# Performance work log

Measured on AMD Instinct MI355X. Metric: run time of the kernel, lower is better.

Reference implementation:

```python
import jax, jax.numpy as jnp
import numpy as np

NUM_BINS = 20
EMBED_DIM = 768
NUM_CODES = 1000
BATCH = 131072
EPS = 1e-8


def setup_inputs() -> dict:
    key = jax.random.key(0)
    k1, k2, k3, k4 = jax.random.split(key, 4)
    values = jax.random.uniform(k1, (BATCH,), dtype=jnp.float32)
    code_ids = jax.random.randint(k2, (BATCH,), 0, NUM_CODES, dtype=jnp.int32)
    # per-code sorted quantile boundaries, shape (NUM_CODES, NUM_BINS-1)
    boundaries = jnp.sort(
        jax.random.uniform(k3, (NUM_CODES, NUM_BINS - 1), dtype=jnp.float32), axis=1
    )
    embed_table = jax.random.normal(k4, (NUM_BINS, EMBED_DIM), dtype=jnp.float32)
    return {
        "values": values,
        "code_ids": code_ids,
        "boundaries": boundaries,
        "embed_table": embed_table,
    }


def reference(values, code_ids, boundaries, embed_table):
    nb = embed_table.shape[0]  # num_bins
    # gather each sample's boundary row: (B, nb-1)
    brows = boundaries[code_ids]
    # torch.searchsorted default == side='left'
    idx = jax.vmap(jnp.searchsorted)(brows, values)
    idx = jnp.clip(idx, 0, nb - 1)
    interior = (idx > 0) & (idx < nb - 1)
    # boundary gathers (clipped so edge rows stay in range; masked out below)
    lo_b = jnp.take_along_axis(brows, jnp.clip(idx - 1, 0, nb - 2)[:, None], axis=1)[:, 0]
    hi_b = jnp.take_along_axis(brows, jnp.clip(idx, 0, nb - 2)[:, None], axis=1)[:, 0]
    denom = hi_b - lo_b
    tiny = jnp.abs(denom) < EPS
    safe_denom = jnp.where(tiny, 1.0, denom)
    alpha = jnp.where(tiny, 0.5, jnp.clip((values - lo_b) / safe_denom, 0.0, 1.0))
    # at edge bins the original returns a single bin embedding (alpha irrelevant)
    alpha = jnp.where(interior, alpha, 0.0)
    lower_idx = jnp.where(idx == 0, 0, jnp.where(idx >= nb - 1, nb - 1, idx - 1))
    upper_idx = jnp.where(interior, idx, lower_idx)
    a = alpha[:, None]
    out = (1.0 - a) * embed_table[lower_idx] + a * embed_table[upper_idx]
    return out  # (B, EMBED_DIM)
```

## Files before the change

kernel.cpp:

```cpp
#include <hip/hip_runtime.h>
#include <cfloat>

#define NB      20
#define NBOUND  19
#define ED      768
#define ED4     192
#define EPS     1e-8f

__global__ __launch_bounds__(256) void sde_kernel(
    const float* __restrict__ values,
    const int*   __restrict__ code_ids,
    const float* __restrict__ boundaries,
    const float* __restrict__ embed_table,
    float*       __restrict__ out,
    int batch)
{
    const int wave = blockIdx.x * (blockDim.x >> 6) + (threadIdx.x >> 6);
    const int lane = threadIdx.x & 63;
    if (wave >= batch) return;
    const int b = wave;

    const float v = values[b];
    const int   c = code_ids[b];

    float bnd = FLT_MAX;
    if (lane < NBOUND) bnd = boundaries[(size_t)c * NBOUND + lane];

    const unsigned long long lt = __ballot(bnd < v);
    const int idx = __popcll(lt);

    int lo_i = idx - 1; lo_i = lo_i < 0 ? 0 : lo_i;
    int hi_i = idx > NBOUND - 1 ? NBOUND - 1 : idx;
    const float lo_b = __shfl(bnd, lo_i);
    const float hi_b = __shfl(bnd, hi_i);

    const bool interior = (idx > 0) && (idx < NB - 1);
    const float denom = hi_b - lo_b;
    const bool tiny = fabsf(denom) < EPS;

    float alpha = (v - lo_b) / (tiny ? 1.0f : denom);
    alpha = fminf(fmaxf(alpha, 0.0f), 1.0f);
    if (tiny)      alpha = 0.5f;
    if (!interior) alpha = 0.0f;

    const int lower = (idx == 0) ? 0 : ((idx >= NB - 1) ? NB - 1 : idx - 1);
    const int upper = interior ? idx : lower;

    const float4* __restrict__ tlo = (const float4*)(embed_table + (size_t)lower * ED);
    const float4* __restrict__ thi = (const float4*)(embed_table + (size_t)upper * ED);
    float4* __restrict__ orow = (float4*)(out + (size_t)b * ED);

    const float om = 1.0f - alpha;
    #pragma unroll
    for (int k = 0; k < 3; ++k) {
        const int s = lane + k * 64;
        const float4 e0 = tlo[s];
        const float4 e1 = thi[s];
        float4 r;
        r.x = om * e0.x + alpha * e1.x;
        r.y = om * e0.y + alpha * e1.y;
        r.z = om * e0.z + alpha * e1.z;
        r.w = om * e0.w + alpha * e1.w;
        orow[s] = r;
    }
}

extern "C" void kernel_launch(void* const* d_in, const int* in_sizes, int n_in,
                              void* d_out, int out_size, void* d_ws, size_t ws_size,
                              hipStream_t stream)
{
    const float* values     = (const float*)d_in[0];
    const int*   code_ids   = (const int*)  d_in[1];
    const float* boundaries = (const float*)d_in[2];
    const float* embed      = (const float*)d_in[3];
    float*       out        = (float*)d_out;

    const int batch = in_sizes[0];
    const int waves_per_block = 4;
    const int blocks = (batch + waves_per_block - 1) / waves_per_block;

    sde_kernel<<<blocks, 256, 0, stream>>>(values, code_ids, boundaries, embed, out, batch);
}
```

Before: 409.3 us.

## Split bin search into per-thread kernel and add nontemporal interpolation writes

Splits the work into two kernels. The first does the bucket search with one thread per sample and writes a compact alpha and index record to workspace. The second uses one wave per row to do the interpolation and writes the output with nontemporal stores. This removes the per-row ballot, shuffle and scattered boundary load from the bandwidth-bound write kernel, at the cost of an extra launch and a workspace round trip. If no workspace is given, the original fused kernel runs instead.

```diff
diff --git a/kernel.cpp b/kernel.cpp
--- a/kernel.cpp
+++ b/kernel.cpp
@@ -4,8 +4,84 @@
 #define NB      20
 #define NBOUND  19
 #define ED      768
-#define ED4     192
 #define EPS     1e-8f
+
+typedef float vf4 __attribute__((ext_vector_type(4)));
+
+__global__ __launch_bounds__(256) void sde_search(
+    const float* __restrict__ values,
+    const int*   __restrict__ code_ids,
+    const float* __restrict__ boundaries,
+    uint2*       __restrict__ recs,
+    int batch)
+{
+    const int i = blockIdx.x * 256 + threadIdx.x;
+    if (i >= batch) return;
+
+    const float v = values[i];
+    const int   c = code_ids[i];
+    const float* __restrict__ br = boundaries + (size_t)c * NBOUND;
+
+    int idx = 0;
+    #pragma unroll
+    for (int j = 0; j < NBOUND; ++j) idx += (br[j] < v) ? 1 : 0;
+
+    int lo_i = idx - 1; lo_i = lo_i < 0 ? 0 : lo_i;
+    int hi_i = idx > NBOUND - 1 ? NBOUND - 1 : idx;
+    const float lo_b = br[lo_i];
+    const float hi_b = br[hi_i];
+
+    const bool interior = (idx > 0) && (idx < NB - 1);
+    const float denom = hi_b - lo_b;
+    const bool tiny = fabsf(denom) < EPS;
+
+    float alpha = (v - lo_b) / (tiny ? 1.0f : denom);
+    alpha = fminf(fmaxf(alpha, 0.0f), 1.0f);
+    if (tiny)      alpha = 0.5f;
+    if (!interior) alpha = 0.0f;
+
+    const int lower = (idx == 0) ? 0 : ((idx >= NB - 1) ? NB - 1 : idx - 1);
+    const int upper = interior ? idx : lower;
+
+    uint2 r;
+    r.x = __float_as_uint(alpha);
+    r.y = (unsigned)lower | ((unsigned)upper << 8);
+    recs[i] = r;
+}
+
+__global__ __launch_bounds__(256) void sde_interp(
+    const uint2* __restrict__ recs,
+    const float* __restrict__ embed_table,
+    float*       __restrict__ out,
+    int batch)
+{
+    const int wave = blockIdx.x * (blockDim.x >> 6) + (threadIdx.x >> 6);
+    const int lane = threadIdx.x & 63;
+    if (wave >= batch) return;
+
+    const uint2 rec = recs[wave];
+    const float alpha = __uint_as_float(rec.x);
+    const int   lower = (int)(rec.y & 0xffu);
+    const int   upper = (int)((rec.y >> 8) & 0xffu);
+
+    const vf4* __restrict__ tlo = (const vf4*)(embed_table + (size_t)lower * ED);
+    const vf4* __restrict__ thi = (const vf4*)(embed_table + (size_t)upper * ED);
+    vf4* __restrict__ orow = (vf4*)(out + (size_t)wave * ED);
+
+    const float om = 1.0f - alpha;
+    #pragma unroll
+    for (int k = 0; k < 3; ++k) {
+        const int s = lane + k * 64;
+        const vf4 e0 = tlo[s];
+        const vf4 e1 = thi[s];
+        vf4 r;
+        r.x = om * e0.x + alpha * e1.x;
+        r.y = om * e0.y + alpha * e1.y;
+        r.z = om * e0.z + alpha * e1.z;
+        r.w = om * e0.w + alpha * e1.w;
+        __builtin_nontemporal_store(r, &orow[s]);
+    }
+}
 
 __global__ __launch_bounds__(256) void sde_kernel(
     const float* __restrict__ values,
@@ -76,8 +152,18 @@
     float*       out        = (float*)d_out;
 
     const int batch = in_sizes[0];
-    const int waves_per_block = 4;
-    const int blocks = (batch + waves_per_block - 1) / waves_per_block;
 
-    sde_kernel<<<blocks, 256, 0, stream>>>(values, code_ids, boundaries, embed, out, batch);
+    if (d_ws != nullptr && ws_size >= (size_t)batch * sizeof(uint2)) {
+        uint2* recs = (uint2*)d_ws;
+        const int blocksA = (batch + 255) / 256;
+        sde_search<<<blocksA, 256, 0, stream>>>(values, code_ids, boundaries, recs, batch);
+
+        const int waves_per_block = 4;
+        const int blocksB = (batch + waves_per_block - 1) / waves_per_block;
+        sde_interp<<<blocksB, 256, 0, stream>>>(recs, embed, out, batch);
+    } else {
+        const int waves_per_block = 4;
+        const int blocks = (batch + waves_per_block - 1) / waves_per_block;
+        sde_kernel<<<blocks, 256, 0, stream>>>(values, code_ids, boundaries, embed, out, batch);
+    }
 }
```

Measured after the change: 396.5 us. 1.03x faster.
